# Performance work log

Hardware: AMD Instinct MI355X
Metric: run time of the kernel (lower is better)

The kernel has to match this reference:

```python
import jax, jax.numpy as jnp
from jax import lax
import numpy as np

B, H, W = 1024, 28, 28
EPS = 1e-5


def _conv(x, w, b):
    # 3x3, stride 1, pad 1, NCHW/OIHW
    y = lax.conv_general_dilated(x, w, (1, 1), ((1, 1), (1, 1)),
                                 dimension_numbers=('NCHW', 'OIHW', 'NCHW'))
    return y + b[None, :, None, None]


def _bn(x, g, b, m, v):
    # inference-mode batchnorm (affine with running stats)
    s = (g * lax.rsqrt(v + EPS))[None, :, None, None]
    return (x - m[None, :, None, None]) * s + b[None, :, None, None]


def _deform_sample(x, off):
    # x: [B,C,H,W], off: [B,18,H,W] ordered (y,x) per 3x3 tap
    Bs, C, Hs, Ws = x.shape
    off = off.reshape(Bs, 9, 2, Hs, Ws)
    k = jnp.arange(3, dtype=x.dtype) - 1.0
    ky = jnp.repeat(k, 3)  # [9]
    kx = jnp.tile(k, 3)    # [9]
    py = jnp.arange(Hs, dtype=x.dtype)[None, None, :, None] + ky[None, :, None, None] + off[:, :, 0]
    px = jnp.arange(Ws, dtype=x.dtype)[None, None, None, :] + kx[None, :, None, None] + off[:, :, 1]
    y0 = jnp.floor(py)
    x0 = jnp.floor(px)
    y1 = y0 + 1.0
    x1 = x0 + 1.0
    wy1 = py - y0
    wy0 = 1.0 - wy1
    wx1 = px - x0
    wx0 = 1.0 - wx1
    flat = x.reshape(Bs, C, Hs * Ws)

    def gather(yy, xx):
        valid = (yy >= 0) & (yy <= Hs - 1) & (xx >= 0) & (xx <= Ws - 1)
        yc = jnp.clip(yy, 0, Hs - 1).astype(jnp.int32)
        xc = jnp.clip(xx, 0, Ws - 1).astype(jnp.int32)
        idx = (yc * Ws + xc).reshape(Bs, -1)  # [B, 9*H*W]
        g = jax.vmap(lambda f, i: f[:, i])(flat, idx)  # [B, C, 9*H*W]
        return g.reshape(Bs, C, 9, Hs, Ws) * valid[:, None].astype(x.dtype)

    s = (gather(y0, x0) * (wy0 * wx0)[:, None]
         + gather(y0, x1) * (wy0 * wx1)[:, None]
         + gather(y1, x0) * (wy1 * wx0)[:, None]
         + gather(y1, x1) * (wy1 * wx1)[:, None])
    return s  # [B, C, 9, H, W]


def setup_inputs() -> dict:
    key = jax.random.key(0)
    ks = jax.random.split(key, 16)

    def rn(k, shape, s=0.05):
        return jax.random.normal(k, shape, jnp.float32) * s

    inp = {
        'x': jax.random.normal(ks[0], (B, 1, H, W), jnp.float32),
        'w_off': rn(ks[1], (18, 1, 3, 3)),
        'b_off': jnp.zeros((18,), jnp.float32),
        'w_dcn': rn(ks[2], (32, 1, 3, 3), 0.3),
        'b_dcn': rn(ks[3], (32,)),
        'w2': rn(ks[4], (64, 32, 3, 3), 0.06),
        'b2': rn(ks[5], (64,)),
        'w3': rn(ks[6], (128, 64, 3, 3), 0.04),
        'b3': rn(ks[7], (128,)),
        'w4': rn(ks[8], (128, 128, 3, 3), 0.03),
        'b4': rn(ks[9], (128,)),
        'w_fc': rn(ks[10], (10, 128), 0.09),
        'b_fc': rn(ks[11], (10,)),
    }
    chans = {'bn1': 32, 'bn2': 64, 'bn3': 128, 'bn4': 128}
    for i, (n, c) in enumerate(chans.items()):
        kk = jax.random.split(ks[12 + i], 4)
        inp[n + '_g'] = 1.0 + rn(kk[0], (c,), 0.1)
        inp[n + '_b'] = rn(kk[1], (c,), 0.1)
        inp[n + '_m'] = rn(kk[2], (c,), 0.1)
        inp[n + '_v'] = jax.random.uniform(kk[3], (c,), jnp.float32, 0.5, 1.5)
    return inp


def reference(x, w_off, b_off, w_dcn, b_dcn,
              bn1_g, bn1_b, bn1_m, bn1_v,
              w2, b2, bn2_g, bn2_b, bn2_m, bn2_v,
              w3, b3, bn3_g, bn3_b, bn3_m, bn3_v,
              w4, b4, bn4_g, bn4_b, bn4_m, bn4_v,
              w_fc, b_fc):
    off = _conv(x, w_off, b_off)                      # [B,18,H,W]
    s = _deform_sample(x, off)                        # [B,1,9,H,W]
    h = jnp.einsum('bckhw,ock->bohw', s, w_dcn.reshape(32, 1, 9))
    h = h + b_dcn[None, :, None, None]
    h = _bn(h, bn1_g, bn1_b, bn1_m, bn1_v)
    h = _bn(jax.nn.relu(_conv(h, w2, b2)), bn2_g, bn2_b, bn2_m, bn2_v)
    h = _bn(jax.nn.relu(_conv(h, w3, b3)), bn3_g, bn3_b, bn3_m, bn3_v)
    h = _bn(jax.nn.relu(_conv(h, w4, b4)), bn4_g, bn4_b, bn4_m, bn4_v)
    pooled = h.mean(axis=(2, 3))                      # avg_pool k=28 == global mean
    logits = pooled @ w_fc.T + b_fc
    return jax.nn.log_softmax(logits, axis=1)
```

## Files before the change

kernel.cpp:

```cpp
#include <hip/hip_runtime.h>
#include <hip/hip_bf16.h>

typedef __bf16 bf16x8 __attribute__((ext_vector_type(8)));
typedef float  f32x4  __attribute__((ext_vector_type(4)));

#define BN_EPS 1e-5f

constexpr size_t ACT_PER_IMG = 57600 + 115200 + 230400;
constexpr size_t SZ_POOL = (size_t)1024 * 128 * 4;
constexpr size_t SZ_W2   = (size_t)9 * 64 * 32 * 2;
constexpr size_t SZ_W3   = (size_t)9 * 128 * 64 * 2;
constexpr size_t SZ_W4   = (size_t)9 * 128 * 128 * 2;
constexpr size_t SZ_BN   = 704 * 4;
constexpr size_t SZ_FIXED = SZ_POOL + SZ_W2 + SZ_W3 + SZ_W4 + SZ_BN;

__device__ __forceinline__ unsigned pack2(float a, float b) {
    __hip_bfloat162 h = __float22bfloat162_rn(make_float2(a, b));
    union { __hip_bfloat162 h2; unsigned u; } u;
    u.h2 = h;
    return u.u;
}

struct PrepArgs {
    const float *w2, *w3, *w4;
    const float *g1, *b1, *m1, *v1;
    const float *g2, *b2, *m2, *v2;
    const float *g3, *b3, *m3, *v3;
    const float *g4, *b4, *m4, *v4;
    __hip_bfloat16 *W2, *W3, *W4;
    float *bn;
};

__global__ __launch_bounds__(256) void prep_k(PrepArgs a) {
    int idx = blockIdx.x * 256 + threadIdx.x;
    if (idx < 18432) {
        int e = idx & 7, lane = (idx >> 3) & 63, r = idx >> 9;
        int nb = r & 3, t = r >> 2;
        int o = nb * 16 + (lane & 15);
        int i = (lane >> 4) * 8 + e;
        a.W2[idx] = __float2bfloat16(a.w2[(o * 32 + i) * 9 + t]);
        return;
    }
    idx -= 18432;
    if (idx < 73728) {
        int e = idx & 7, lane = (idx >> 3) & 63, r = idx >> 9;
        int nb = r & 7, s = r >> 3;
        int kc = s & 1, t = s >> 1;
        int o = nb * 16 + (lane & 15);
        int i = kc * 32 + (lane >> 4) * 8 + e;
        a.W3[idx] = __float2bfloat16(a.w3[(o * 64 + i) * 9 + t]);
        return;
    }
    idx -= 73728;
    if (idx < 147456) {
        int e = idx & 7, lane = (idx >> 3) & 63, r = idx >> 9;
        int nb = r & 7, s = r >> 3;
        int kc = s & 3, t = s >> 2;
        int o = nb * 16 + (lane & 15);
        int i = kc * 32 + (lane >> 4) * 8 + e;
        a.W4[idx] = __float2bfloat16(a.w4[(o * 128 + i) * 9 + t]);
        return;
    }
    idx -= 147456;
    if (idx < 352) {
        const float *g, *bb, *mm, *vv; int c, so, cn;
        if (idx < 32)       { g = a.g1; bb = a.b1; mm = a.m1; vv = a.v1; c = idx;       so = 0;   cn = 32;  }
        else if (idx < 96)  { g = a.g2; bb = a.b2; mm = a.m2; vv = a.v2; c = idx - 32;  so = 64;  cn = 64;  }
        else if (idx < 224) { g = a.g3; bb = a.b3; mm = a.m3; vv = a.v3; c = idx - 96;  so = 192; cn = 128; }
        else                { g = a.g4; bb = a.b4; mm = a.m4; vv = a.v4; c = idx - 224; so = 448; cn = 128; }
        float s = g[c] * rsqrtf(vv[c] + BN_EPS);
        a.bn[so + c] = s;
        a.bn[so + cn + c] = bb[c] - mm[c] * s;
    }
}

__global__ __launch_bounds__(256) void deform_k(
    const float* __restrict__ x, const float* __restrict__ w_off,
    const float* __restrict__ b_off, const float* __restrict__ w_dcn,
    const float* __restrict__ b_dcn, const float* __restrict__ bn,
    __hip_bfloat16* __restrict__ act1, __hip_bfloat16* __restrict__ act2,
    __hip_bfloat16* __restrict__ act3, float* __restrict__ pooled, int b0)
{
    const int lb = blockIdx.x;
    const int b  = b0 + lb;
    const int tid = threadIdx.x;
    __shared__ float xp[900];
    __shared__ float sw[564];
    float* swo = sw;
    float* sbo = sw + 162;
    float* swd = sw + 180;
    float* sbd = sw + 468;
    float* ss1 = sw + 500;
    float* ssh = sw + 532;

    for (int i = tid; i < 900; i += 256) {
        int y = i / 30, xc = i % 30;
        float v = 0.f;
        if (y >= 1 && y <= 28 && xc >= 1 && xc <= 28)
            v = x[(size_t)b * 784 + (y - 1) * 28 + (xc - 1)];
        xp[i] = v;
    }
    for (int i = tid; i < 564; i += 256) {
        float v;
        if (i < 162)      v = w_off[i];
        else if (i < 180) v = b_off[i - 162];
        else if (i < 468) v = w_dcn[i - 180];
        else if (i < 500) v = b_dcn[i - 468];
        else if (i < 532) v = bn[i - 500];
        else              v = bn[32 + (i - 532)];
        sw[i] = v;
    }
    if (tid < 128) pooled[b * 128 + tid] = 0.f;
    __syncthreads();

    for (int p = tid; p < 784; p += 256) {
        int y = p / 28, xx = p % 28;
        float off[18];
        #pragma unroll
        for (int o = 0; o < 18; o++) off[o] = sbo[o];
        #pragma unroll
        for (int ty = 0; ty < 3; ty++)
            #pragma unroll
            for (int tx = 0; tx < 3; tx++) {
                float xv = xp[(y + ty) * 30 + (xx + tx)];
                int tap = ty * 3 + tx;
                #pragma unroll
                for (int o = 0; o < 18; o++) off[o] = fmaf(xv, swo[o * 9 + tap], off[o]);
            }
        float s[9];
        #pragma unroll
        for (int j = 0; j < 9; j++) {
            float py = (float)y + (float)(j / 3 - 1) + off[2 * j];
            float px = (float)xx + (float)(j % 3 - 1) + off[2 * j + 1];
            float y0 = floorf(py), x0 = floorf(px);
            float wy1 = py - y0, wx1 = px - x0;
            float wy0 = 1.f - wy1, wx0 = 1.f - wx1;
            float acc = 0.f;
            #pragma unroll
            for (int cy = 0; cy < 2; cy++)
                #pragma unroll
                for (int cx = 0; cx < 2; cx++) {
                    float yy = y0 + (float)cy, xf = x0 + (float)cx;
                    bool valid = (yy >= 0.f) && (yy <= 27.f) && (xf >= 0.f) && (xf <= 27.f);
                    int yc = (int)fminf(fmaxf(yy, 0.f), 27.f);
                    int xc = (int)fminf(fmaxf(xf, 0.f), 27.f);
                    float g = valid ? xp[(yc + 1) * 30 + (xc + 1)] : 0.f;
                    float w = (cy ? wy1 : wy0) * (cx ? wx1 : wx0);
                    acc = fmaf(g, w, acc);
                }
            s[j] = acc;
        }
        size_t base = ((size_t)lb * 900 + (size_t)(y + 1) * 30 + (xx + 1)) * 32;
        #pragma unroll
        for (int c0 = 0; c0 < 32; c0 += 8) {
            float h[8];
            #pragma unroll
            for (int ci = 0; ci < 8; ci++) {
                int c = c0 + ci;
                float hv = sbd[c];
                #pragma unroll
                for (int j = 0; j < 9; j++) hv = fmaf(s[j], swd[c * 9 + j], hv);
                h[ci] = hv * ss1[c] + ssh[c];
            }
            uint4 q;
            q.x = pack2(h[0], h[1]); q.y = pack2(h[2], h[3]);
            q.z = pack2(h[4], h[5]); q.w = pack2(h[6], h[7]);
            *reinterpret_cast<uint4*>(&act1[base + c0]) = q;
        }
    }

    for (int i = tid; i < 116; i += 256) {
        int py, px;
        if (i < 30)      { py = 0;          px = i; }
        else if (i < 60) { py = 29;         px = i - 30; }
        else if (i < 88) { py = i - 60 + 1; px = 0; }
        else             { py = i - 88 + 1; px = 29; }
        size_t pix = (size_t)lb * 900 + (size_t)py * 30 + px;
        uint4 z = {0, 0, 0, 0};
        uint4* p1 = reinterpret_cast<uint4*>(&act1[pix * 32]);
        #pragma unroll
        for (int k = 0; k < 4; k++) p1[k] = z;
        uint4* p2 = reinterpret_cast<uint4*>(&act2[pix * 64]);
        #pragma unroll
        for (int k = 0; k < 8; k++) p2[k] = z;
        uint4* p3 = reinterpret_cast<uint4*>(&act3[pix * 128]);
        #pragma unroll
        for (int k = 0; k < 16; k++) p3[k] = z;
    }
}

template<int CIN>
__device__ __forceinline__ int swz(int ofs) {
    if constexpr (CIN == 128) return (ofs >> 4) & 0x70;
    else if constexpr (CIN == 64) return (ofs >> 3) & 0x70;
    else return (ofs >> 2) & 0x30;
}

template<int COUT, int NFW>
__device__ __forceinline__ void loadWf(const __hip_bfloat16* __restrict__ Wt,
                                       int s, int nhalf, int lane, bf16x8 (&bf)[NFW]) {
    constexpr int NB = COUT / 16;
    #pragma unroll
    for (int nf = 0; nf < NFW; ++nf)
        bf[nf] = *reinterpret_cast<const bf16x8*>(
            Wt + (((size_t)s * NB + nhalf * NFW + nf) * 64 + lane) * 8);
}

template<int CIN, int MFW>
__device__ __forceinline__ void loadAf(const __hip_bfloat16* tile,
                                       int s, const int (&pr)[4], const int (&pc)[4],
                                       int kg, bf16x8 (&af)[MFW]) {
    constexpr int KC = CIN / 32;
    int t = s / KC, kc = (s % KC) * 32;
    int ty = t / 3, tx = t % 3;
    #pragma unroll
    for (int mf = 0; mf < MFW; ++mf) {
        int pix = (pr[mf] + ty) * 30 + (pc[mf] + tx);
        int ba = (pix * CIN + kc + kg * 8) * 2;
        ba ^= swz<CIN>(ba);
        af[mf] = *reinterpret_cast<const bf16x8*>(
            reinterpret_cast<const char*>(tile) + ba);
    }
}

template<int MFW, int NFW>
__device__ __forceinline__ void mstep(const bf16x8 (&af)[MFW], const bf16x8 (&wf)[NFW],
                                      f32x4 (&acc)[MFW][NFW]) {
    #pragma unroll
    for (int mf = 0; mf < MFW; ++mf)
        #pragma unroll
        for (int nf = 0; nf < NFW; ++nf)
            acc[mf][nf] = __builtin_amdgcn_mfma_f32_16x16x32_bf16(
                af[mf], wf[nf], acc[mf][nf], 0, 0, 0);
}

template<int CIN, int COUT, bool POOL, int MFW>
__device__ __forceinline__ void conv_body(
    const __hip_bfloat16* tile,
    const __hip_bfloat16* __restrict__ Wt,
    const float* __restrict__ bconv, const float* __restrict__ bnS,
    const float* __restrict__ bnB, __hip_bfloat16* __restrict__ aout,
    float* __restrict__ pooled, int lb, int gb, int rg, int lane, int mhalf, int nhalf)
{
    constexpr int KC  = CIN / 32;
    constexpr int NS  = 9 * KC;
    constexpr int NFW = COUT / 32;
    const int l15 = lane & 15, kg = lane >> 4;
    const int nbase = nhalf * (NFW * 16) + l15;

    int pr[4], pc[4];
    #pragma unroll
    for (int mf = 0; mf < MFW; ++mf) {
        int m = (mhalf * 4 + mf) * 16 + l15;
        pr[mf] = m / 28;
        pc[mf] = m % 28;
    }

    f32x4 acc[MFW][NFW] = {};
    bf16x8 wA[NFW], wB[NFW], wC[NFW];
    bf16x8 aA[MFW], aB[MFW], aC[MFW];

    loadWf<COUT, NFW>(Wt, 0, nhalf, lane, wA);
    loadAf<CIN, MFW>(tile, 0, pr, pc, kg, aA);
    loadWf<COUT, NFW>(Wt, 1, nhalf, lane, wB);
    loadAf<CIN, MFW>(tile, 1, pr, pc, kg, aB);

    #pragma unroll
    for (int s = 0; s < NS; s += 3) {
        if (s + 2 < NS) {
            loadWf<COUT, NFW>(Wt, s + 2, nhalf, lane, wC);
            loadAf<CIN, MFW>(tile, s + 2, pr, pc, kg, aC);
        }
        __builtin_amdgcn_sched_barrier(0);
        mstep<MFW, NFW>(aA, wA, acc);
        if (s + 3 < NS) {
            loadWf<COUT, NFW>(Wt, s + 3, nhalf, lane, wA);
            loadAf<CIN, MFW>(tile, s + 3, pr, pc, kg, aA);
        }
        __builtin_amdgcn_sched_barrier(0);
        mstep<MFW, NFW>(aB, wB, acc);
        if (s + 4 < NS) {
            loadWf<COUT, NFW>(Wt, s + 4, nhalf, lane, wB);
            loadAf<CIN, MFW>(tile, s + 4, pr, pc, kg, aB);
        }
        __builtin_amdgcn_sched_barrier(0);
        if (s + 2 < NS) mstep<MFW, NFW>(aC, wC, acc);
    }

    if constexpr (!POOL) {
        #pragma unroll
        for (int mf = 0; mf < MFW; ++mf) {
            #pragma unroll
            for (int nf = 0; nf < NFW; ++nf) {
                int n = nbase + nf * 16;
                float bc = bconv[n], sc = bnS[n], sh = bnB[n];
                #pragma unroll
                for (int r = 0; r < 4; r++) {
                    int m = (mhalf * 4 + mf) * 16 + kg * 4 + r;
                    float y = acc[mf][nf][r] + bc;
                    y = fmaxf(y, 0.f);
                    y = y * sc + sh;
                    int oy = m / 28, ox = m % 28;
                    aout[((size_t)lb * 900 + (size_t)(rg * 4 + oy + 1) * 30 + (ox + 1)) * COUT + n]
                        = __float2bfloat16(y);
                }
            }
        }
    } else {
        #pragma unroll
        for (int nf = 0; nf < NFW; ++nf) {
            int n = nbase + nf * 16;
            float bc = bconv[n], sc = bnS[n], sh = bnB[n];
            float ps = 0.f;
            #pragma unroll
            for (int mf = 0; mf < MFW; ++mf)
                #pragma unroll
                for (int r = 0; r < 4; r++) {
                    float y = acc[mf][nf][r] + bc;
                    y = fmaxf(y, 0.f);
                    ps += y * sc + sh;
                }
            ps += __shfl_xor(ps, 16, 64);
            ps += __shfl_xor(ps, 32, 64);
            if (lane < 16) atomicAdd(&pooled[gb * COUT + n], ps);
        }
    }
}

template<int CIN, int COUT, bool POOL>
__global__ __launch_bounds__(256, 2) void conv_k(
    const __hip_bfloat16* __restrict__ ain,
    const __hip_bfloat16* __restrict__ Wt,
    const float* __restrict__ bconv,
    const float* __restrict__ bnS,
    const float* __restrict__ bnB,
    __hip_bfloat16* __restrict__ aout,
    float* __restrict__ pooled, int b0, int nimg)
{
    __shared__ __align__(16) __hip_bfloat16 tile[180 * CIN];
    const int tid = threadIdx.x;
    const int lane = tid & 63;
    const int wv = tid >> 6;
    const int mhalf = wv >> 1, nhalf = wv & 1;

    int rg, lb;
    {
        int flat = blockIdx.x + 7 * blockIdx.y;
        if ((nimg & 7) == 0) {
            int xcd = flat & 7, idx = flat >> 3;
            lb = xcd * (nimg >> 3) + idx / 7;
            rg = idx % 7;
        } else {
            rg = blockIdx.x; lb = blockIdx.y;
        }
    }

    const char* src = reinterpret_cast<const char*>(
        ain + ((size_t)lb * 900 + (size_t)rg * 120) * CIN);
    constexpr int TB = 180 * CIN * 2;
    for (int ofs = tid * 16; ofs < TB; ofs += 4096) {
        uint4 v = *reinterpret_cast<const uint4*>(src + ofs);
        *reinterpret_cast<uint4*>(reinterpret_cast<char*>(tile) + (ofs ^ swz<CIN>(ofs))) = v;
    }
    __syncthreads();

    if (mhalf == 0)
        conv_body<CIN, COUT, POOL, 4>(tile, Wt, bconv, bnS, bnB, aout, pooled,
                                      lb, b0 + lb, rg, lane, mhalf, nhalf);
    else
        conv_body<CIN, COUT, POOL, 3>(tile, Wt, bconv, bnS, bnB, aout, pooled,
                                      lb, b0 + lb, rg, lane, mhalf, nhalf);
}

__global__ __launch_bounds__(256) void head_k(
    const float* __restrict__ pooled, const float* __restrict__ wfc,
    const float* __restrict__ bfc, float* __restrict__ out)
{
    int b = blockIdx.x * 4 + (threadIdx.x >> 6);
    int lane = threadIdx.x & 63;
    float m0 = pooled[b * 128 + lane] * (1.f / 784.f);
    float m1 = pooled[b * 128 + 64 + lane] * (1.f / 784.f);
    float lg[10];
    #pragma unroll
    for (int k = 0; k < 10; k++) {
        float p = m0 * wfc[k * 128 + lane] + m1 * wfc[k * 128 + 64 + lane];
        #pragma unroll
        for (int s2 = 32; s2 >= 1; s2 >>= 1) p += __shfl_xor(p, s2, 64);
        lg[k] = p + bfc[k];
    }
    float mx = lg[0];
    #pragma unroll
    for (int k = 1; k < 10; k++) mx = fmaxf(mx, lg[k]);
    float se = 0.f;
    #pragma unroll
    for (int k = 0; k < 10; k++) se += expf(lg[k] - mx);
    float lse = mx + logf(se);
    #pragma unroll
    for (int k = 0; k < 10; k++)
        if (lane == k) out[b * 10 + k] = lg[k] - lse;
}

extern "C" void kernel_launch(void* const* d_in, const int* in_sizes, int n_in,
                              void* d_out, int out_size, void* d_ws, size_t ws_size,
                              hipStream_t stream) {
    (void)in_sizes; (void)n_in; (void)out_size;
    const float* x     = (const float*)d_in[0];
    const float* w_off = (const float*)d_in[1];
    const float* b_off = (const float*)d_in[2];
    const float* w_dcn = (const float*)d_in[3];
    const float* b_dcn = (const float*)d_in[4];
    const float* w2    = (const float*)d_in[5];
    const float* b2    = (const float*)d_in[6];
    const float* w3    = (const float*)d_in[7];
    const float* b3    = (const float*)d_in[8];
    const float* w4    = (const float*)d_in[9];
    const float* b4    = (const float*)d_in[10];
    const float* w_fc  = (const float*)d_in[11];
    const float* b_fc  = (const float*)d_in[12];

    int CH = 256;
    while (CH > 1 && (size_t)CH * ACT_PER_IMG + SZ_FIXED > ws_size) CH >>= 1;
    const int NCHUNK = 1024 / CH;

    char* ws = (char*)d_ws;
    const size_t szA1 = (size_t)CH * 57600;
    const size_t szA2 = (size_t)CH * 115200;
    const size_t szA3 = (size_t)CH * 230400;
    __hip_bfloat16* act1 = (__hip_bfloat16*)(ws);
    __hip_bfloat16* act2 = (__hip_bfloat16*)(ws + szA1);
    __hip_bfloat16* act3 = (__hip_bfloat16*)(ws + szA1 + szA2);
    float* pooled        = (float*)(ws + szA1 + szA2 + szA3);
    __hip_bfloat16* W2   = (__hip_bfloat16*)(ws + szA1 + szA2 + szA3 + SZ_POOL);
    __hip_bfloat16* W3   = (__hip_bfloat16*)((char*)W2 + SZ_W2);
    __hip_bfloat16* W4   = (__hip_bfloat16*)((char*)W3 + SZ_W3);
    float* bn            = (float*)((char*)W4 + SZ_W4);

    PrepArgs pa;
    pa.w2 = w2; pa.w3 = w3; pa.w4 = w4;
    pa.g1 = (const float*)d_in[13]; pa.b1 = (const float*)d_in[14];
    pa.m1 = (const float*)d_in[15]; pa.v1 = (const float*)d_in[16];
    pa.g2 = (const float*)d_in[17]; pa.b2 = (const float*)d_in[18];
    pa.m2 = (const float*)d_in[19]; pa.v2 = (const float*)d_in[20];
    pa.g3 = (const float*)d_in[21]; pa.b3 = (const float*)d_in[22];
    pa.m3 = (const float*)d_in[23]; pa.v3 = (const float*)d_in[24];
    pa.g4 = (const float*)d_in[25]; pa.b4 = (const float*)d_in[26];
    pa.m4 = (const float*)d_in[27]; pa.v4 = (const float*)d_in[28];
    pa.W2 = W2; pa.W3 = W3; pa.W4 = W4; pa.bn = bn;

    prep_k<<<938, 256, 0, stream>>>(pa);
    for (int c = 0; c < NCHUNK; ++c) {
        int b0 = c * CH;
        deform_k<<<CH, 256, 0, stream>>>(x, w_off, b_off, w_dcn, b_dcn, bn,
                                         act1, act2, act3, pooled, b0);
        conv_k<32, 64, false><<<dim3(7, CH), 256, 0, stream>>>(
            act1, W2, b2, bn + 64, bn + 128, act2, nullptr, b0, CH);
        conv_k<64, 128, false><<<dim3(7, CH), 256, 0, stream>>>(
            act2, W3, b3, bn + 192, bn + 320, act3, nullptr, b0, CH);
        conv_k<128, 128, true><<<dim3(7, CH), 256, 0, stream>>>(
            act3, W4, b4, bn + 448, bn + 576, nullptr, pooled, b0, CH);
    }
    head_k<<<256, 256, 0, stream>>>(pooled, w_fc, b_fc, (float*)d_out);
}
```

Baseline: 656.2 us.

## Use two-wave conv blocks with full 7-fragment M tiles for conv2 and conv3

Adds a 128-thread conv kernel variant where each of two waves computes all 112 output pixels of the row-group tile against half the output channels. It replaces the 4-wave 4/3 M-split for the first two 3x3 convs, so each loaded A fragment feeds more MFMAs and each weight fragment is reused across 7 M fragments. The pipeline is double-buffered rather than triple-buffered. The larger accumulator and fragment arrays raise register pressure, and fewer waves per block may reduce latency hiding and the bandwidth of the tile load.

New measurement: 625.6 us. -4.7%, faster.

```diff
diff --git a/kernel.cpp b/kernel.cpp
--- a/kernel.cpp
+++ b/kernel.cpp
@@ -198,18 +198,18 @@
 
 template<int COUT, int NFW>
 __device__ __forceinline__ void loadWf(const __hip_bfloat16* __restrict__ Wt,
-                                       int s, int nhalf, int lane, bf16x8 (&bf)[NFW]) {
+                                       int s, int ng, int lane, bf16x8 (&bf)[NFW]) {
     constexpr int NB = COUT / 16;
     #pragma unroll
     for (int nf = 0; nf < NFW; ++nf)
         bf[nf] = *reinterpret_cast<const bf16x8*>(
-            Wt + (((size_t)s * NB + nhalf * NFW + nf) * 64 + lane) * 8);
+            Wt + (((size_t)s * NB + ng * NFW + nf) * 64 + lane) * 8);
 }
 
 template<int CIN, int MFW>
-__device__ __forceinline__ void loadAf(const __hip_bfloat16* tile,
-                                       int s, const int (&pr)[4], const int (&pc)[4],
-                                       int kg, bf16x8 (&af)[MFW]) {
+__device__ __forceinline__ void loadAf4(const __hip_bfloat16* tile,
+                                        int s, const int (&pr)[4], const int (&pc)[4],
+                                        int kg, bf16x8 (&af)[MFW]) {
     constexpr int KC = CIN / 32;
     int t = s / KC, kc = (s % KC) * 32;
     int ty = t / 3, tx = t % 3;
@@ -235,7 +235,7 @@
 }
 
 template<int CIN, int COUT, bool POOL, int MFW>
-__device__ __forceinline__ void conv_body(
+__device__ __forceinline__ void conv_body4(
     const __hip_bfloat16* tile,
     const __hip_bfloat16* __restrict__ Wt,
     const float* __restrict__ bconv, const float* __restrict__ bnS,
@@ -261,27 +261,27 @@
     bf16x8 aA[MFW], aB[MFW], aC[MFW];
 
     loadWf<COUT, NFW>(Wt, 0, nhalf, lane, wA);
-    loadAf<CIN, MFW>(tile, 0, pr, pc, kg, aA);
+    loadAf4<CIN, MFW>(tile, 0, pr, pc, kg, aA);
     loadWf<COUT, NFW>(Wt, 1, nhalf, lane, wB);
-    loadAf<CIN, MFW>(tile, 1, pr, pc, kg, aB);
+    loadAf4<CIN, MFW>(tile, 1, pr, pc, kg, aB);
 
     #pragma unroll
     for (int s = 0; s < NS; s += 3) {
         if (s + 2 < NS) {
             loadWf<COUT, NFW>(Wt, s + 2, nhalf, lane, wC);
-            loadAf<CIN, MFW>(tile, s + 2, pr, pc, kg, aC);
+            loadAf4<CIN, MFW>(tile, s + 2, pr, pc, kg, aC);
         }
         __builtin_amdgcn_sched_barrier(0);
         mstep<MFW, NFW>(aA, wA, acc);
         if (s + 3 < NS) {
             loadWf<COUT, NFW>(Wt, s + 3, nhalf, lane, wA);
-            loadAf<CIN, MFW>(tile, s + 3, pr, pc, kg, aA);
+            loadAf4<CIN, MFW>(tile, s + 3, pr, pc, kg, aA);
         }
         __builtin_amdgcn_sched_barrier(0);
         mstep<MFW, NFW>(aB, wB, acc);
         if (s + 4 < NS) {
             loadWf<COUT, NFW>(Wt, s + 4, nhalf, lane, wB);
-            loadAf<CIN, MFW>(tile, s + 4, pr, pc, kg, aB);
+            loadAf4<CIN, MFW>(tile, s + 4, pr, pc, kg, aB);
         }
         __builtin_amdgcn_sched_barrier(0);
         if (s + 2 < NS) mstep<MFW, NFW>(aC, wC, acc);
@@ -328,7 +328,7 @@
 }
 
 template<int CIN, int COUT, bool POOL>
-__global__ __launch_bounds__(256, 2) void conv_k(
+__global__ __launch_bounds__(256, 2) void conv_k4(
     const __hip_bfloat16* __restrict__ ain,
     const __hip_bfloat16* __restrict__ Wt,
     const float* __restrict__ bconv,
@@ -365,11 +365,167 @@
     __syncthreads();
 
     if (mhalf == 0)
-        conv_body<CIN, COUT, POOL, 4>(tile, Wt, bconv, bnS, bnB, aout, pooled,
-                                      lb, b0 + lb, rg, lane, mhalf, nhalf);
+        conv_body4<CIN, COUT, POOL, 4>(tile, Wt, bconv, bnS, bnB, aout, pooled,
+                                       lb, b0 + lb, rg, lane, mhalf, nhalf);
     else
-        conv_body<CIN, COUT, POOL, 3>(tile, Wt, bconv, bnS, bnB, aout, pooled,
-                                      lb, b0 + lb, rg, lane, mhalf, nhalf);
+        conv_body4<CIN, COUT, POOL, 3>(tile, Wt, bconv, bnS, bnB, aout, pooled,
+                                       lb, b0 + lb, rg, lane, mhalf, nhalf);
+}
+
+template<int CIN>
+__device__ __forceinline__ void loadAf7(const __hip_bfloat16* tile,
+                                        int s, const int (&pr)[7], const int (&pc)[7],
+                                        int kg, bf16x8 (&af)[7]) {
+    constexpr int KC = CIN / 32;
+    int t = s / KC, kc = (s % KC) * 32;
+    int ty = t / 3, tx = t % 3;
+    #pragma unroll
+    for (int mf = 0; mf < 7; ++mf) {
+        int pix = (pr[mf] + ty) * 30 + (pc[mf] + tx);
+        int ba = (pix * CIN + kc + kg * 8) * 2;
+        ba ^= swz<CIN>(ba);
+        af[mf] = *reinterpret_cast<const bf16x8*>(
+            reinterpret_cast<const char*>(tile) + ba);
+    }
+}
+
+template<int NFW>
+__device__ __forceinline__ void mstep7(const bf16x8 (&af)[7], const bf16x8 (&wf)[NFW],
+                                       f32x4 (&acc)[7][NFW]) {
+    #pragma unroll
+    for (int mf = 0; mf < 7; ++mf)
+        #pragma unroll
+        for (int nf = 0; nf < NFW; ++nf)
+            acc[mf][nf] = __builtin_amdgcn_mfma_f32_16x16x32_bf16(
+                af[mf], wf[nf], acc[mf][nf], 0, 0, 0);
+}
+
+template<int CIN, int COUT, bool POOL>
+__device__ __forceinline__ void conv_body2(
+    const __hip_bfloat16* tile,
+    const __hip_bfloat16* __restrict__ Wt,
+    const float* __restrict__ bconv, const float* __restrict__ bnS,
+    const float* __restrict__ bnB, __hip_bfloat16* __restrict__ aout,
+    float* __restrict__ pooled, int lb, int gb, int rg, int lane, int nq)
+{
+    constexpr int KC  = CIN / 32;
+    constexpr int NS  = 9 * KC;
+    constexpr int NFW = COUT / 32;
+    const int l15 = lane & 15, kg = lane >> 4;
+    const int nbase = nq * (NFW * 16) + l15;
+
+    int pr[7], pc[7];
+    #pragma unroll
+    for (int mf = 0; mf < 7; ++mf) {
+        int m = mf * 16 + l15;
+        pr[mf] = m / 28;
+        pc[mf] = m % 28;
+    }
+
+    f32x4 acc[7][NFW] = {};
+    bf16x8 wA[NFW], wB[NFW], aA[7], aB[7];
+
+    loadWf<COUT, NFW>(Wt, 0, nq, lane, wA);
+    loadAf7<CIN>(tile, 0, pr, pc, kg, aA);
+    loadWf<COUT, NFW>(Wt, 1, nq, lane, wB);
+    loadAf7<CIN>(tile, 1, pr, pc, kg, aB);
+
+    #pragma unroll
+    for (int s = 0; s < NS; s += 2) {
+        __builtin_amdgcn_sched_barrier(0);
+        mstep7<NFW>(aA, wA, acc);
+        if (s + 2 < NS) {
+            loadWf<COUT, NFW>(Wt, s + 2, nq, lane, wA);
+            loadAf7<CIN>(tile, s + 2, pr, pc, kg, aA);
+        }
+        __builtin_amdgcn_sched_barrier(0);
+        if (s + 1 < NS) {
+            mstep7<NFW>(aB, wB, acc);
+            if (s + 3 < NS) {
+                loadWf<COUT, NFW>(Wt, s + 3, nq, lane, wB);
+                loadAf7<CIN>(tile, s + 3, pr, pc, kg, aB);
+            }
+        }
+    }
+
+    if constexpr (!POOL) {
+        #pragma unroll
+        for (int mf = 0; mf < 7; ++mf) {
+            #pragma unroll
+            for (int nf = 0; nf < NFW; ++nf) {
+                int n = nbase + nf * 16;
+                float bc = bconv[n], sc = bnS[n], sh = bnB[n];
+                #pragma unroll
+                for (int r = 0; r < 4; r++) {
+                    int m = mf * 16 + kg * 4 + r;
+                    float y = acc[mf][nf][r] + bc;
+                    y = fmaxf(y, 0.f);
+                    y = y * sc + sh;
+                    int oy = m / 28, ox = m % 28;
+                    aout[((size_t)lb * 900 + (size_t)(rg * 4 + oy + 1) * 30 + (ox + 1)) * COUT + n]
+                        = __float2bfloat16(y);
+                }
+            }
+        }
+    } else {
+        #pragma unroll
+        for (int nf = 0; nf < NFW; ++nf) {
+            int n = nbase + nf * 16;
+            float bc = bconv[n], sc = bnS[n], sh = bnB[n];
+            float ps = 0.f;
+            #pragma unroll
+            for (int mf = 0; mf < 7; ++mf)
+                #pragma unroll
+                for (int r = 0; r < 4; r++) {
+                    float y = acc[mf][nf][r] + bc;
+                    y = fmaxf(y, 0.f);
+                    ps += y * sc + sh;
+                }
+            ps += __shfl_xor(ps, 16, 64);
+            ps += __shfl_xor(ps, 32, 64);
+            if (lane < 16) atomicAdd(&pooled[gb * COUT + n], ps);
+        }
+    }
+}
+
+template<int CIN, int COUT, bool POOL>
+__global__ __launch_bounds__(128, 2) void conv_k2(
+    const __hip_bfloat16* __restrict__ ain,
+    const __hip_bfloat16* __restrict__ Wt,
+    const float* __restrict__ bconv,
+    const float* __restrict__ bnS,
+    const float* __restrict__ bnB,
+    __hip_bfloat16* __restrict__ aout,
+    float* __restrict__ pooled, int b0, int nimg)
+{
+    __shared__ __align__(16) __hip_bfloat16 tile[180 * CIN];
+    const int tid = threadIdx.x;
+    const int lane = tid & 63;
+    const int nq = tid >> 6;
+
+    int rg, lb;
+    {
+        int flat = blockIdx.x + 7 * blockIdx.y;
+        if ((nimg & 7) == 0) {
+            int xcd = flat & 7, idx = flat >> 3;
+            lb = xcd * (nimg >> 3) + idx / 7;
+            rg = idx % 7;
+        } else {
+            rg = blockIdx.x; lb = blockIdx.y;
+        }
+    }
+
+    const char* src = reinterpret_cast<const char*>(
+        ain + ((size_t)lb * 900 + (size_t)rg * 120) * CIN);
+    constexpr int TB = 180 * CIN * 2;
+    for (int ofs = tid * 16; ofs < TB; ofs += 2048) {
+        uint4 v = *reinterpret_cast<const uint4*>(src + ofs);
+        *reinterpret_cast<uint4*>(reinterpret_cast<char*>(tile) + (ofs ^ swz<CIN>(ofs))) = v;
+    }
+    __syncthreads();
+
+    conv_body2<CIN, COUT, POOL>(tile, Wt, bconv, bnS, bnB, aout, pooled,
+                                lb, b0 + lb, rg, lane, nq);
 }
 
 __global__ __launch_bounds__(256) void head_k(
@@ -452,11 +608,11 @@
         int b0 = c * CH;
         deform_k<<<CH, 256, 0, stream>>>(x, w_off, b_off, w_dcn, b_dcn, bn,
                                          act1, act2, act3, pooled, b0);
-        conv_k<32, 64, false><<<dim3(7, CH), 256, 0, stream>>>(
+        conv_k2<32, 64, false><<<dim3(7, CH), 128, 0, stream>>>(
             act1, W2, b2, bn + 64, bn + 128, act2, nullptr, b0, CH);
-        conv_k<64, 128, false><<<dim3(7, CH), 256, 0, stream>>>(
+        conv_k2<64, 128, false><<<dim3(7, CH), 128, 0, stream>>>(
             act2, W3, b3, bn + 192, bn + 320, act3, nullptr, b0, CH);
-        conv_k<128, 128, true><<<dim3(7, CH), 256, 0, stream>>>(
+        conv_k4<128, 128, true><<<dim3(7, CH), 256, 0, stream>>>(
             act3, W4, b4, bn + 448, bn + 576, nullptr, pooled, b0, CH);
     }
     head_k<<<256, 256, 0, stream>>>(pooled, w_fc, b_fc, (float*)d_out);
```
